# Performance work log

Hardware: AMD Instinct MI355X
Metric: run time of the kernel (lower is better)

The kernel has to match this reference:

```python
import jax, jax.numpy as jnp
import numpy as np
from jax import lax

B, T, U, H, INNER, V = 4, 200, 100, 320, 512, 1000
BLANK = 0


def setup_inputs() -> dict:
    key = jax.random.key(0)
    ks = jax.random.split(key, 8)
    enc_state = jax.random.normal(ks[0], (B, T, H), dtype=jnp.float32)
    dec_state = jax.random.normal(ks[1], (B, U + 1, H), dtype=jnp.float32)
    tokens = jax.random.randint(ks[2], (B, U), 1, V, dtype=jnp.int32)
    output_length = jnp.full((B,), T, dtype=jnp.int32)
    tokens_length = jnp.full((B,), U, dtype=jnp.int32)
    s1 = 1.0 / np.sqrt(2 * H)
    s2 = 1.0 / np.sqrt(INNER)
    W1 = jax.random.uniform(ks[3], (2 * H, INNER), minval=-s1, maxval=s1, dtype=jnp.float32)
    b1 = jax.random.uniform(ks[4], (INNER,), minval=-s1, maxval=s1, dtype=jnp.float32)
    W2 = jax.random.uniform(ks[5], (INNER, V), minval=-s2, maxval=s2, dtype=jnp.float32)
    b2 = jax.random.uniform(ks[6], (V,), minval=-s2, maxval=s2, dtype=jnp.float32)
    return {"enc_state": enc_state, "dec_state": dec_state, "tokens": tokens,
            "output_length": output_length, "tokens_length": tokens_length,
            "W1": W1, "b1": b1, "W2": W2, "b2": b2}


def joint_logits(enc_state, dec_state, W1, b1, W2, b2):
    # concat joint: cat(enc[b,t], dec[b,u]) @ W1 == enc @ W1[:H] + dec @ W1[H:]
    h_enc = jnp.einsum('bth,hi->bti', enc_state, W1[:H])      # (B,T,INNER)
    h_dec = jnp.einsum('buh,hi->bui', dec_state, W1[H:])      # (B,U+1,INNER)
    h = jnp.tanh(h_enc[:, :, None, :] + h_dec[:, None, :, :] + b1)  # (B,T,U+1,INNER)
    return jnp.einsum('btui,iv->btuv', h, W2) + b2            # (B,T,U+1,V)


def rnnt_loss(log_probs, tokens, output_length, tokens_length):
    # log_probs: (B,T,U+1,V); tokens: (B,U) int
    Bn, Tn, U1, _ = log_probs.shape
    blank_lp = log_probs[..., BLANK]                           # (B,T,U+1)
    label_lp = jnp.take_along_axis(
        log_probs[:, :, :U1 - 1, :],
        tokens[:, None, :, None].astype(jnp.int32).repeat(Tn, axis=1),
        axis=-1)[..., 0]                                       # (B,T,U)

    # row t=0: alpha[0,u] = sum_{u'<u} label_lp[0,u']
    def row0_step(c, a):
        n = c + a
        return n, n
    init0 = jnp.zeros((Bn,), dtype=log_probs.dtype)
    _, rest0 = lax.scan(row0_step, init0, label_lp[:, 0, :].T)  # (U,B)
    alpha0 = jnp.concatenate([init0[None], rest0], axis=0).T    # (B,U+1)

    def t_step(alpha_prev, xs):
        blank_prev, label_t = xs                # (B,U+1), (B,U)
        b = alpha_prev + blank_prev             # blank transition from row t-1
        def u_step(c, inp):
            b_u, a_prev = inp
            n = jnp.logaddexp(b_u, c + a_prev)
            return n, n
        first = b[:, 0]
        _, rest = lax.scan(u_step, first, (b[:, 1:].T, label_t.T))
        alpha_t = jnp.concatenate([first[None], rest], axis=0).T
        return alpha_t, alpha_t

    xs = (blank_lp[:, :-1, :].transpose(1, 0, 2), label_lp[:, 1:, :].transpose(1, 0, 2))
    _, alphas = lax.scan(t_step, alpha0, xs)                    # (T-1,B,U+1)
    alpha = jnp.concatenate([alpha0[None], alphas], axis=0).transpose(1, 0, 2)  # (B,T,U+1)

    bidx = jnp.arange(Bn)
    t_idx = output_length - 1
    u_idx = tokens_length
    ll = alpha[bidx, t_idx, u_idx] + blank_lp[bidx, t_idx, u_idx]
    return -jnp.mean(ll)


def reference(enc_state, dec_state, tokens, output_length, tokens_length, W1, b1, W2, b2):
    logits = joint_logits(enc_state, dec_state, W1, b1, W2, b2)
    log_probs = jax.nn.log_softmax(logits, axis=-1)
    return rnnt_loss(log_probs, tokens, output_length, tokens_length)
```

## Files before the change

### kernel.cpp

```cpp
#include <hip/hip_runtime.h>
#include <hip/hip_bf16.h>

#define T_DIM 200
#define U_DIM 100
#define U1    101
#define H_DIM 320
#define K_INNER 512
#define V_DIM 1000
#define B_DIM 4
#define DP_PITCH 128
#define ND 300
#define ROWS 48

typedef unsigned short ushort_t;
typedef unsigned int uint32;

typedef short bfrag8 __attribute__((ext_vector_type(8)));
typedef float ffrag4 __attribute__((ext_vector_type(4)));

#define LOG2E 1.4426950408889634f
#define LN2   0.6931471805599453f

__device__ __forceinline__ uint32 pk_bf16(float a, float b) {
  __hip_bfloat162 h = __float22bfloat162_rn(make_float2(a, b));
  return *(uint32*)&h;
}

__device__ __forceinline__ float tanh_fast(float x) {
  float e = __expf(2.0f * x);
  return 1.0f - __fdividef(2.0f, e + 1.0f);
}

__global__ __launch_bounds__(512)
void prep_kernel(const float* __restrict__ enc, const float* __restrict__ dec,
                 const float* __restrict__ W1, const float* __restrict__ W2,
                 float* __restrict__ hEnc, float* __restrict__ hDec,
                 ushort_t* __restrict__ W2f)
{
  __shared__ union { float sIn[8][H_DIM]; float sW[8][1024]; } sh;
  const int tid = threadIdx.x;
  const int blk = blockIdx.x;

  if (blk < 151) {
    const float* inp; float* outp; int nRows, rowOff, b0;
    if (blk < 100) { inp = enc; outp = hEnc; nRows = B_DIM * T_DIM; rowOff = 0;     b0 = blk; }
    else           { inp = dec; outp = hDec; nRows = B_DIM * U1;    rowOff = H_DIM; b0 = blk - 100; }
    const int r0 = b0 * 8;
    for (int i = tid; i < 8 * H_DIM; i += 512) {
      int r = i / H_DIM, k = i - r * H_DIM;
      int rr = r0 + r;
      sh.sIn[r][k] = (rr < nRows) ? inp[(size_t)rr * H_DIM + k] : 0.0f;
    }
    __syncthreads();
    const int c = tid;
    float acc[8];
#pragma unroll
    for (int r = 0; r < 8; ++r) acc[r] = 0.0f;
    const float* Wp = W1 + (size_t)rowOff * K_INNER + c;
    for (int k = 0; k < H_DIM; k += 4) {
      float w0 = Wp[(size_t)(k + 0) * K_INNER];
      float w1 = Wp[(size_t)(k + 1) * K_INNER];
      float w2 = Wp[(size_t)(k + 2) * K_INNER];
      float w3 = Wp[(size_t)(k + 3) * K_INNER];
#pragma unroll
      for (int r = 0; r < 8; ++r) {
        float4 s = *(const float4*)&sh.sIn[r][k];
        acc[r] = fmaf(s.w, w3, fmaf(s.z, w2, fmaf(s.y, w1, fmaf(s.x, w0, acc[r]))));
      }
    }
#pragma unroll
    for (int r = 0; r < 8; ++r) {
      int rr = r0 + r;
      if (rr < nRows) outp[(size_t)rr * K_INNER + c] = acc[r];
    }
  } else {
    const int kc = blk - 151;
    for (int i = tid; i < 8 * 1024; i += 512) {
      int r = i >> 10, n = i & 1023;
      sh.sW[r][n] = (n < V_DIM) ? W2[(size_t)(kc * 8 + r) * V_DIM + n] : 0.0f;
    }
    __syncthreads();
#pragma unroll
    for (int h = 0; h < 2; ++h) {
      int n = tid + h * 512;
      uint4 pk;
      pk.x = pk_bf16(sh.sW[0][n], sh.sW[1][n]);
      pk.y = pk_bf16(sh.sW[2][n], sh.sW[3][n]);
      pk.z = pk_bf16(sh.sW[4][n], sh.sW[5][n]);
      pk.w = pk_bf16(sh.sW[6][n], sh.sW[7][n]);
      *(uint4*)&W2f[((size_t)kc * 1024 + n) * 8] = pk;
    }
  }
}

__global__ __launch_bounds__(256, 3)
void joint_kernel(const float* __restrict__ hEnc, const float* __restrict__ hDec,
                  const float* __restrict__ b1, const ushort_t* __restrict__ W2f,
                  const float* __restrict__ b2, const int* __restrict__ tokens,
                  float* __restrict__ blankD, float* __restrict__ labelD)
{
  __shared__ union SU {
    ushort_t X[ROWS * K_INNER];
    float red[4][ROWS][4];
  } sh;

  const int tid = threadIdx.x;
  const int b  = blockIdx.z;
  const int t0 = blockIdx.y * 12;
  const int u0 = blockIdx.x * 4;

  for (int i = tid; i < ROWS * 64; i += 256) {
    const int row = i >> 6;
    const int G = i & 63;
    const int tcl = min(t0 + (row >> 2), T_DIM - 1);
    const int ucl = min(u0 + (row & 3), U1 - 1);
    const float* er = hEnc + (size_t)(b * T_DIM + tcl) * K_INNER;
    const float* dr = hDec + (size_t)(b * U1 + ucl) * K_INNER;
    const int k = G << 3;
    float4 e0 = *(const float4*)(er + k);
    float4 e1 = *(const float4*)(er + k + 4);
    float4 d0 = *(const float4*)(dr + k);
    float4 d1 = *(const float4*)(dr + k + 4);
    float4 c0 = *(const float4*)(b1 + k);
    float4 c1 = *(const float4*)(b1 + k + 4);
    uint4 pk;
    pk.x = pk_bf16(tanh_fast(e0.x + d0.x + c0.x), tanh_fast(e0.y + d0.y + c0.y));
    pk.y = pk_bf16(tanh_fast(e0.z + d0.z + c0.z), tanh_fast(e0.w + d0.w + c0.w));
    pk.z = pk_bf16(tanh_fast(e1.x + d1.x + c1.x), tanh_fast(e1.y + d1.y + c1.y));
    pk.w = pk_bf16(tanh_fast(e1.z + d1.z + c1.z), tanh_fast(e1.w + d1.w + c1.w));
    const int slot = (G + row) & 63;
    *(uint4*)&sh.X[row * K_INNER + (slot << 3)] = pk;
  }
  __syncthreads();

  const int wave = tid >> 6;
  const int lane = tid & 63;
  const int l15 = lane & 15;
  const int quad = lane >> 4;

  float sumexp[3][4], labelA[3][4], blankV[3][4];
#pragma unroll
  for (int i = 0; i < 3; ++i)
#pragma unroll
    for (int j = 0; j < 4; ++j) { sumexp[i][j] = 0.0f; labelA[i][j] = 0.0f; blankV[i][j] = 0.0f; }

  int tokv[4];
#pragma unroll
  for (int j = 0; j < 4; ++j)
    tokv[j] = (u0 + j < U_DIM) ? tokens[b * U_DIM + u0 + j] : -1;

#pragma unroll 1
  for (int ct = 0; ct < 4; ++ct) {
    const int nbase = ct * 256 + wave * 64;
    ffrag4 acc[3][4];
    ffrag4 zero4 = {0.0f, 0.0f, 0.0f, 0.0f};
#pragma unroll
    for (int rb = 0; rb < 3; ++rb)
#pragma unroll
      for (int cb = 0; cb < 4; ++cb) acc[rb][cb] = zero4;

#pragma unroll 4
    for (int ks = 0; ks < 16; ++ks) {
      const int kchunk = ks * 4 + quad;
      bfrag8 av[3];
#pragma unroll
      for (int rb = 0; rb < 3; ++rb) {
        const int m = rb * 16 + l15;
        const int slot = (kchunk + m) & 63;
        av[rb] = *(const bfrag8*)&sh.X[m * K_INNER + (slot << 3)];
      }
      bfrag8 bv[4];
#pragma unroll
      for (int cb = 0; cb < 4; ++cb) {
        const int n = nbase + cb * 16 + l15;
        bv[cb] = *(const bfrag8*)(W2f + ((size_t)kchunk * 1024 + n) * 8);
      }
#pragma unroll
      for (int rb = 0; rb < 3; ++rb)
#pragma unroll
        for (int cb = 0; cb < 4; ++cb)
          acc[rb][cb] = __builtin_amdgcn_mfma_f32_16x16x32_bf16(av[rb], bv[cb], acc[rb][cb], 0, 0, 0);
    }

#pragma unroll
    for (int cb = 0; cb < 4; ++cb) {
      const int v = nbase + cb * 16 + l15;
      const float b2v = (v < V_DIM) ? b2[v] : -1e30f;
      const float b2s = b2v * LOG2E;
#pragma unroll
      for (int rb = 0; rb < 3; ++rb)
#pragma unroll
        for (int reg = 0; reg < 4; ++reg) {
          float a = acc[rb][cb][reg];
          sumexp[rb][reg] += exp2f(fmaf(a, LOG2E, b2s));
          labelA[rb][reg] += (v == tokv[reg]) ? a : 0.0f;
        }
    }
    if (nbase == 0) {
#pragma unroll
      for (int rb = 0; rb < 3; ++rb)
#pragma unroll
        for (int reg = 0; reg < 4; ++reg) blankV[rb][reg] = acc[rb][0][reg];
    }
  }

#pragma unroll
  for (int mask = 1; mask <= 8; mask <<= 1) {
#pragma unroll
    for (int rb = 0; rb < 3; ++rb)
#pragma unroll
      for (int reg = 0; reg < 4; ++reg) {
        sumexp[rb][reg] += __shfl_xor(sumexp[rb][reg], mask, 64);
        labelA[rb][reg] += __shfl_xor(labelA[rb][reg], mask, 64);
      }
  }

  __syncthreads();
  if (l15 == 0) {
#pragma unroll
    for (int rb = 0; rb < 3; ++rb)
#pragma unroll
      for (int reg = 0; reg < 4; ++reg) {
        int row = rb * 16 + quad * 4 + reg;
        sh.red[wave][row][0] = sumexp[rb][reg];
        sh.red[wave][row][1] = blankV[rb][reg];
        sh.red[wave][row][2] = labelA[rb][reg];
      }
  }
  __syncthreads();
  if (tid < ROWS) {
    float S  = sh.red[0][tid][0] + sh.red[1][tid][0] + sh.red[2][tid][0] + sh.red[3][tid][0];
    float Bl = sh.red[0][tid][1] + sh.red[1][tid][1] + sh.red[2][tid][1] + sh.red[3][tid][1];
    float Lb = sh.red[0][tid][2] + sh.red[1][tid][2] + sh.red[2][tid][2] + sh.red[3][tid][2];
    int t = t0 + (tid >> 2);
    int u = u0 + (tid & 3);
    if (t < T_DIM && u < U1) {
      float lse2 = __log2f(S);
      int tok = (u < U_DIM) ? tokens[b * U_DIM + u] : 0;
      int d = t + u;
      size_t idx = ((size_t)b * ND + d) * DP_PITCH + u;
      blankD[idx] = (Bl + b2[0])   * LOG2E - lse2;
      labelD[idx] = (Lb + b2[tok]) * LOG2E - lse2;
    }
  }
}

__global__ __launch_bounds__(256)
void dp_kernel(const float* __restrict__ blankD, const float* __restrict__ labelD,
               const int* __restrict__ outLen, const int* __restrict__ tokLen,
               float* __restrict__ outLoss)
{
  __shared__ float llsh[B_DIM];
  const int tid = threadIdx.x;
  const int wv = tid >> 6;
  const int lane = tid & 63;
  const float* bD = blankD + (size_t)wv * ND * DP_PITCH;
  const float* lD = labelD + (size_t)wv * ND * DP_PITCH;
  const int tIdx = outLen[wv] - 1;
  const int uIdx = tokLen[wv];
  const int dStar = tIdx + uIdx;
  const float NEG = -1e30f;

  float aE = (lane == 0) ? 0.0f : NEG;
  float aO = NEG;
  float ll2 = 0.0f;
  if (dStar == 0 && lane == 0) ll2 = bD[0];

  const int uE = 2 * lane, uO = uE + 1;

#define LDB(dg) (*(const float2*)&bD[(size_t)(dg) * DP_PITCH + uE])
#define LDL(dg) (*(const float2*)&lD[(size_t)(dg) * DP_PITCH + uE])

  float2 B0 = LDB(0), L0 = LDL(0);
  float2 B1 = LDB(1), L1 = LDL(1);
  float2 B2 = LDB(2), L2 = LDL(2);
  float2 B3 = LDB(3), L3 = LDL(3);

#define DPSTEP(d, Bv, Lv)                                                    \
  {                                                                          \
    float aO_up = __shfl_up(aO, 1, 64);                                      \
    if (lane == 0) aO_up = NEG;                                              \
    float labUp = __shfl_up(Lv.y, 1, 64);                                    \
    float bt0 = aE + Bv.x, lt0 = aO_up + labUp;                              \
    float mx0 = fmaxf(bt0, lt0), mn0 = fminf(bt0, lt0);                      \
    float r0 = mx0 + __log2f(1.0f + exp2f(mn0 - mx0));                       \
    int te = (d) - uE;                                                       \
    float nE = ((uE <= U_DIM) && (te >= 0) && (te < T_DIM)) ? r0 : NEG;      \
    float bt1 = aO + Bv.y, lt1 = aE + Lv.x;                                  \
    float mx1 = fmaxf(bt1, lt1), mn1 = fminf(bt1, lt1);                      \
    float r1 = mx1 + __log2f(1.0f + exp2f(mn1 - mx1));                       \
    int to = (d) - uO;                                                       \
    float nO = ((uO <= U_DIM) && (to >= 0) && (to < T_DIM)) ? r1 : NEG;      \
    aE = nE; aO = nO;                                                        \
    if ((d) == dStar) {                                                      \
      float blk = bD[(size_t)(d) * DP_PITCH + uIdx];                         \
      if (uIdx == uE)      ll2 = nE + blk;                                   \
      else if (uIdx == uO) ll2 = nO + blk;                                   \
    }                                                                        \
  }

  for (int base = 1; base <= 293; base += 4) {
    DPSTEP(base + 0, B0, L0); B0 = LDB(base + 3); L0 = LDL(base + 3);
    DPSTEP(base + 1, B1, L1); B1 = LDB(base + 4); L1 = LDL(base + 4);
    DPSTEP(base + 2, B2, L2); B2 = LDB(base + 5); L2 = LDL(base + 5);
    DPSTEP(base + 3, B3, L3); B3 = LDB(base + 6); L3 = LDL(base + 6);
  }
  DPSTEP(297, B0, L0);
  DPSTEP(298, B1, L1);
  DPSTEP(299, B2, L2);

#undef DPSTEP
#undef LDB
#undef LDL

#pragma unroll
  for (int mask = 1; mask < 64; mask <<= 1) ll2 += __shfl_xor(ll2, mask, 64);
  if (lane == 0) llsh[wv] = ll2;
  __syncthreads();
  if (tid == 0)
    outLoss[0] = -(llsh[0] + llsh[1] + llsh[2] + llsh[3]) * 0.25f * LN2;
}

extern "C" void kernel_launch(void* const* d_in, const int* in_sizes, int n_in,
                              void* d_out, int out_size, void* d_ws, size_t ws_size,
                              hipStream_t stream)
{
  const float* enc    = (const float*)d_in[0];
  const float* dec    = (const float*)d_in[1];
  const int*   tokens = (const int*)d_in[2];
  const int*   outLen = (const int*)d_in[3];
  const int*   tokLen = (const int*)d_in[4];
  const float* W1     = (const float*)d_in[5];
  const float* b1     = (const float*)d_in[6];
  const float* W2     = (const float*)d_in[7];
  const float* b2     = (const float*)d_in[8];
  float* out = (float*)d_out;

  char* ws = (char*)d_ws;
  float*    hEnc   = (float*)(ws + 0);
  float*    hDec   = (float*)(ws + 1638400);
  ushort_t* W2f    = (ushort_t*)(ws + 2465792);
  float*    blankD = (float*)(ws + 3514368);
  float*    labelD = (float*)(ws + 4128768);

  prep_kernel<<<dim3(215), dim3(512), 0, stream>>>(enc, dec, W1, W2, hEnc, hDec, W2f);
  joint_kernel<<<dim3(26, 17, B_DIM), dim3(256), 0, stream>>>(hEnc, hDec, b1, W2f, b2, tokens, blankD, labelD);
  dp_kernel<<<dim3(1), dim3(256), 0, stream>>>(blankD, labelD, outLen, tokLen, out);
}
```

Baseline: 272.7 us.

## Switch joint GEMM from bf16 to fp8 MFMA with scaled W2 and deeper DP prefetch

Converts W2 (pre-scaled by 16) and the tanh activations to fp8 and uses the 16x16x32 fp8 MFMA instead of bf16. The logits are rescaled by 1/16 in the softmax and output paths. This halves the operand bytes in LDS and global memory, and the smaller shared buffer allows raising the occupancy hint to 4 blocks. The DP kernel also widens its load prefetch from 4 to 8 steps. The cost is lower numerical precision in the logits, which may hurt loss accuracy.

```diff
diff --git a/kernel.cpp b/kernel.cpp
--- a/kernel.cpp
+++ b/kernel.cpp
@@ -13,13 +13,15 @@
 #define ROWS 48
 
 typedef unsigned short ushort_t;
+typedef unsigned char uchar_t;
 typedef unsigned int uint32;
-
-typedef short bfrag8 __attribute__((ext_vector_type(8)));
+typedef long lfrag;
+
 typedef float ffrag4 __attribute__((ext_vector_type(4)));
 
-#define LOG2E 1.4426950408889634f
-#define LN2   0.6931471805599453f
+#define LOG2E   1.4426950408889634f
+#define LOG2E16 (1.4426950408889634f * 0.0625f)
+#define LN2     0.6931471805599453f
 
 __device__ __forceinline__ uint32 pk_bf16(float a, float b) {
   __hip_bfloat162 h = __float22bfloat162_rn(make_float2(a, b));
@@ -29,13 +31,23 @@
 __device__ __forceinline__ float tanh_fast(float x) {
   float e = __expf(2.0f * x);
   return 1.0f - __fdividef(2.0f, e + 1.0f);
+}
+
+__device__ __forceinline__ uint2 pk_fp8x8(float t0, float t1, float t2, float t3,
+                                          float t4, float t5, float t6, float t7) {
+  uint2 r;
+  r.x = (uint32)__builtin_amdgcn_cvt_pk_fp8_f32(t0, t1, 0, false);
+  r.x = (uint32)__builtin_amdgcn_cvt_pk_fp8_f32(t2, t3, (int)r.x, true);
+  r.y = (uint32)__builtin_amdgcn_cvt_pk_fp8_f32(t4, t5, 0, false);
+  r.y = (uint32)__builtin_amdgcn_cvt_pk_fp8_f32(t6, t7, (int)r.y, true);
+  return r;
 }
 
 __global__ __launch_bounds__(512)
 void prep_kernel(const float* __restrict__ enc, const float* __restrict__ dec,
                  const float* __restrict__ W1, const float* __restrict__ W2,
                  float* __restrict__ hEnc, float* __restrict__ hDec,
-                 ushort_t* __restrict__ W2f)
+                 uchar_t* __restrict__ W2f8)
 {
   __shared__ union { float sIn[8][H_DIM]; float sW[8][1024]; } sh;
   const int tid = threadIdx.x;
@@ -83,24 +95,23 @@
 #pragma unroll
     for (int h = 0; h < 2; ++h) {
       int n = tid + h * 512;
-      uint4 pk;
-      pk.x = pk_bf16(sh.sW[0][n], sh.sW[1][n]);
-      pk.y = pk_bf16(sh.sW[2][n], sh.sW[3][n]);
-      pk.z = pk_bf16(sh.sW[4][n], sh.sW[5][n]);
-      pk.w = pk_bf16(sh.sW[6][n], sh.sW[7][n]);
-      *(uint4*)&W2f[((size_t)kc * 1024 + n) * 8] = pk;
-    }
-  }
-}
-
-__global__ __launch_bounds__(256, 3)
+      uint2 pk = pk_fp8x8(sh.sW[0][n] * 16.f, sh.sW[1][n] * 16.f,
+                          sh.sW[2][n] * 16.f, sh.sW[3][n] * 16.f,
+                          sh.sW[4][n] * 16.f, sh.sW[5][n] * 16.f,
+                          sh.sW[6][n] * 16.f, sh.sW[7][n] * 16.f);
+      *(uint2*)&W2f8[((size_t)kc * 1024 + n) * 8] = pk;
+    }
+  }
+}
+
+__global__ __launch_bounds__(256, 4)
 void joint_kernel(const float* __restrict__ hEnc, const float* __restrict__ hDec,
-                  const float* __restrict__ b1, const ushort_t* __restrict__ W2f,
+                  const float* __restrict__ b1, const uchar_t* __restrict__ W2f8,
                   const float* __restrict__ b2, const int* __restrict__ tokens,
                   float* __restrict__ blankD, float* __restrict__ labelD)
 {
   __shared__ union SU {
-    ushort_t X[ROWS * K_INNER];
+    uchar_t X[ROWS * K_INNER];
     float red[4][ROWS][4];
   } sh;
 
@@ -123,13 +134,12 @@
     float4 d1 = *(const float4*)(dr + k + 4);
     float4 c0 = *(const float4*)(b1 + k);
     float4 c1 = *(const float4*)(b1 + k + 4);
-    uint4 pk;
-    pk.x = pk_bf16(tanh_fast(e0.x + d0.x + c0.x), tanh_fast(e0.y + d0.y + c0.y));
-    pk.y = pk_bf16(tanh_fast(e0.z + d0.z + c0.z), tanh_fast(e0.w + d0.w + c0.w));
-    pk.z = pk_bf16(tanh_fast(e1.x + d1.x + c1.x), tanh_fast(e1.y + d1.y + c1.y));
-    pk.w = pk_bf16(tanh_fast(e1.z + d1.z + c1.z), tanh_fast(e1.w + d1.w + c1.w));
+    uint2 pk = pk_fp8x8(tanh_fast(e0.x + d0.x + c0.x), tanh_fast(e0.y + d0.y + c0.y),
+                        tanh_fast(e0.z + d0.z + c0.z), tanh_fast(e0.w + d0.w + c0.w),
+                        tanh_fast(e1.x + d1.x + c1.x), tanh_fast(e1.y + d1.y + c1.y),
+                        tanh_fast(e1.z + d1.z + c1.z), tanh_fast(e1.w + d1.w + c1.w));
     const int slot = (G + row) & 63;
-    *(uint4*)&sh.X[row * K_INNER + (slot << 3)] = pk;
+    *(uint2*)&sh.X[row * K_INNER + (slot << 3)] = pk;
   }
   __syncthreads();
 
@@ -162,24 +172,24 @@
 #pragma unroll 4
     for (int ks = 0; ks < 16; ++ks) {
       const int kchunk = ks * 4 + quad;
-      bfrag8 av[3];
+      lfrag av[3];
 #pragma unroll
       for (int rb = 0; rb < 3; ++rb) {
         const int m = rb * 16 + l15;
         const int slot = (kchunk + m) & 63;
-        av[rb] = *(const bfrag8*)&sh.X[m * K_INNER + (slot << 3)];
-      }
-      bfrag8 bv[4];
+        av[rb] = *(const lfrag*)&sh.X[m * K_INNER + (slot << 3)];
+      }
+      lfrag bv[4];
 #pragma unroll
       for (int cb = 0; cb < 4; ++cb) {
         const int n = nbase + cb * 16 + l15;
-        bv[cb] = *(const bfrag8*)(W2f + ((size_t)kchunk * 1024 + n) * 8);
+        bv[cb] = *(const lfrag*)(W2f8 + ((size_t)kchunk * 1024 + n) * 8);
       }
 #pragma unroll
       for (int rb = 0; rb < 3; ++rb)
 #pragma unroll
         for (int cb = 0; cb < 4; ++cb)
-          acc[rb][cb] = __builtin_amdgcn_mfma_f32_16x16x32_bf16(av[rb], bv[cb], acc[rb][cb], 0, 0, 0);
+          acc[rb][cb] = __builtin_amdgcn_mfma_f32_16x16x32_fp8_fp8(av[rb], bv[cb], acc[rb][cb], 0, 0, 0);
     }
 
 #pragma unroll
@@ -192,7 +202,7 @@
 #pragma unroll
         for (int reg = 0; reg < 4; ++reg) {
           float a = acc[rb][cb][reg];
-          sumexp[rb][reg] += exp2f(fmaf(a, LOG2E, b2s));
+          sumexp[rb][reg] += exp2f(fmaf(a, LOG2E16, b2s));
           labelA[rb][reg] += (v == tokv[reg]) ? a : 0.0f;
         }
     }
@@ -239,8 +249,8 @@
       int tok = (u < U_DIM) ? tokens[b * U_DIM + u] : 0;
       int d = t + u;
       size_t idx = ((size_t)b * ND + d) * DP_PITCH + u;
-      blankD[idx] = (Bl + b2[0])   * LOG2E - lse2;
-      labelD[idx] = (Lb + b2[tok]) * LOG2E - lse2;
+      blankD[idx] = fmaf(Bl, LOG2E16, b2[0]   * LOG2E) - lse2;
+      labelD[idx] = fmaf(Lb, LOG2E16, b2[tok] * LOG2E) - lse2;
     }
   }
 }
@@ -275,6 +285,10 @@
   float2 B1 = LDB(1), L1 = LDL(1);
   float2 B2 = LDB(2), L2 = LDL(2);
   float2 B3 = LDB(3), L3 = LDL(3);
+  float2 B4 = LDB(4), L4 = LDL(4);
+  float2 B5 = LDB(5), L5 = LDL(5);
+  float2 B6 = LDB(6), L6 = LDL(6);
+  float2 B7 = LDB(7), L7 = LDL(7);
 
 #define DPSTEP(d, Bv, Lv)                                                    \
   {                                                                          \
@@ -299,11 +313,15 @@
     }                                                                        \
   }
 
-  for (int base = 1; base <= 293; base += 4) {
-    DPSTEP(base + 0, B0, L0); B0 = LDB(base + 3); L0 = LDL(base + 3);
-    DPSTEP(base + 1, B1, L1); B1 = LDB(base + 4); L1 = LDL(base + 4);
-    DPSTEP(base + 2, B2, L2); B2 = LDB(base + 5); L2 = LDL(base + 5);
-    DPSTEP(base + 3, B3, L3); B3 = LDB(base + 6); L3 = LDL(base + 6);
+  for (int base = 1; base <= 289; base += 8) {
+    DPSTEP(base + 0, B0, L0); { int dg = min(base + 7,  299); B0 = LDB(dg); L0 = LDL(dg); }
+    DPSTEP(base + 1, B1, L1); { int dg = min(base + 8,  299); B1 = LDB(dg); L1 = LDL(dg); }
+    DPSTEP(base + 2, B2, L2); { int dg = min(base + 9,  299); B2 = LDB(dg); L2 = LDL(dg); }
+    DPSTEP(base + 3, B3, L3); { int dg = min(base + 10, 299); B3 = LDB(dg); L3 = LDL(dg); }
+    DPSTEP(base + 4, B4, L4); { int dg = min(base + 11, 299); B4 = LDB(dg); L4 = LDL(dg); }
+    DPSTEP(base + 5, B5, L5); { int dg = min(base + 12, 299); B5 = LDB(dg); L5 = LDL(dg); }
+    DPSTEP(base + 6, B6, L6); { int dg = min(base + 13, 299); B6 = LDB(dg); L6 = LDL(dg); }
+    DPSTEP(base + 7, B7, L7); { int dg = min(base + 14, 299); B7 = LDB(dg); L7 = LDL(dg); }
   }
   DPSTEP(297, B0, L0);
   DPSTEP(298, B1, L1);
@@ -337,13 +355,13 @@
   float* out = (float*)d_out;
 
   char* ws = (char*)d_ws;
-  float*    hEnc   = (float*)(ws + 0);
-  float*    hDec   = (float*)(ws + 1638400);
-  ushort_t* W2f    = (ushort_t*)(ws + 2465792);
-  float*    blankD = (float*)(ws + 3514368);
-  float*    labelD = (float*)(ws + 4128768);
-
-  prep_kernel<<<dim3(215), dim3(512), 0, stream>>>(enc, dec, W1, W2, hEnc, hDec, W2f);
-  joint_kernel<<<dim3(26, 17, B_DIM), dim3(256), 0, stream>>>(hEnc, hDec, b1, W2f, b2, tokens, blankD, labelD);
+  float*   hEnc   = (float*)(ws + 0);
+  float*   hDec   = (float*)(ws + 1638400);
+  uchar_t* W2f8   = (uchar_t*)(ws + 2465792);
+  float*   blankD = (float*)(ws + 2990080);
+  float*   labelD = (float*)(ws + 3604480);
+
+  prep_kernel<<<dim3(215), dim3(512), 0, stream>>>(enc, dec, W1, W2, hEnc, hDec, W2f8);
+  joint_kernel<<<dim3(26, 17, B_DIM), dim3(256), 0, stream>>>(hEnc, hDec, b1, W2f8, b2, tokens, blankD, labelD);
   dp_kernel<<<dim3(1), dim3(256), 0, stream>>>(blankD, labelD, outLen, tokLen, out);
 }
```

Result: slower. 303.1 us (+11.1%).
